# Optimization experiments

Measured on AMD Instinct MI355X. Metric: run time of the kernel, lower is better.

Reference implementation:

```python
import jax, jax.numpy as jnp
import numpy as np

B, S, DIM, H = 8, 4096, 1024, 16
HD = DIM // H
SCALE = HD ** -0.5


def setup_inputs() -> dict:
    key = jax.random.key(0)
    k1, k2, k3 = jax.random.split(key, 3)
    x = jax.random.normal(k1, (B, S, DIM), dtype=jnp.float32)
    # xavier_uniform-ish scales (exact init irrelevant for correctness baseline)
    Wqkv = jax.random.normal(k2, (DIM, 3 * DIM), dtype=jnp.float32) * (2.0 / (DIM + DIM)) ** 0.5
    bqkv = jnp.zeros((3 * DIM,), dtype=jnp.float32)
    Wproj = jax.random.normal(k3, (DIM, DIM), dtype=jnp.float32) * (2.0 / (DIM + DIM)) ** 0.5
    bproj = jnp.zeros((DIM,), dtype=jnp.float32)
    return {"x": x, "Wqkv": Wqkv, "bqkv": bqkv, "Wproj": Wproj, "bproj": bproj}


def reference(x, Wqkv, bqkv, Wproj, bproj):
    b, s, _ = x.shape
    qkv = x @ Wqkv + bqkv                                  # [b, s, 3*dim]
    qkv = qkv.reshape(b, s, 3, H, HD)
    q, k, v = [jnp.transpose(qkv[:, :, i], (0, 2, 1, 3)) for i in range(3)]  # each [b, h, s, hd]
    q = jax.nn.softmax(q, axis=-2) * SCALE                 # softmax over seqlen
    k = jax.nn.softmax(k, axis=-1)                         # softmax over head_dim
    # original computes (k @ v^T)^T @ q; associativity gives v @ (k^T @ q), O(n*d^2)
    A = jnp.einsum("bhtd,bhte->bhde", k, q)                # [b, h, hd, hd]
    out = jnp.einsum("bhsd,bhde->bhse", v, A)              # [b, h, s, hd]
    out = jnp.transpose(out, (0, 2, 1, 3)).reshape(b, s, DIM)
    return out @ Wproj + bproj
```

## Files before the change

### kernel.cpp

```cpp
#include <hip/hip_runtime.h>
#include <hip/hip_bf16.h>

typedef short s16x8 __attribute__((ext_vector_type(8)));
typedef short s16x4 __attribute__((ext_vector_type(4)));
typedef float f32x4 __attribute__((ext_vector_type(4)));
typedef unsigned int u32x4 __attribute__((ext_vector_type(4)));
typedef unsigned int u32x2 __attribute__((ext_vector_type(2)));

__device__ __forceinline__ float b2f(unsigned short u) {
  unsigned int v = ((unsigned int)u) << 16;
  return __builtin_bit_cast(float, v);
}
__device__ __forceinline__ unsigned short f2b(float f) {
  __hip_bfloat16 h = __float2bfloat16(f);
  return __builtin_bit_cast(unsigned short, h);
}
__device__ __forceinline__ void async_ld16(const unsigned short* g, unsigned short* l) {
  __builtin_amdgcn_global_load_lds(
      (const __attribute__((address_space(1))) void*)g,
      (__attribute__((address_space(3))) void*)l, 16, 0, 0);
}

__global__ __launch_bounds__(256) void cast_x_kernel(const float* __restrict__ x,
                                                     unsigned short* __restrict__ xb) {
  int i = (blockIdx.x * 256 + threadIdx.x) * 4;
  f32x4 v = *(const f32x4*)(x + i);
  u32x2 o;
  o[0] = (unsigned)f2b(v[0]) | ((unsigned)f2b(v[1]) << 16);
  o[1] = (unsigned)f2b(v[2]) | ((unsigned)f2b(v[3]) << 16);
  *(u32x2*)(xb + i) = o;
}

__global__ __launch_bounds__(256) void wtrans_kernel(const float* __restrict__ W,
                                                     unsigned short* __restrict__ Wt,
                                                     int K, int N) {
  __shared__ float tile[64][65];
  int n0 = blockIdx.x * 64, k0 = blockIdx.y * 64;
  int tx = threadIdx.x & 63, ty = threadIdx.x >> 6;
  #pragma unroll
  for (int i = ty; i < 64; i += 4) tile[i][tx] = W[(long)(k0 + i) * N + n0 + tx];
  __syncthreads();
  #pragma unroll
  for (int i = ty; i < 64; i += 4) Wt[(long)(n0 + i) * K + k0 + tx] = f2b(tile[tx][i]);
}

template<bool BF16OUT>
__global__ __launch_bounds__(256) void gemm_bt_kernel(
    const unsigned short* __restrict__ A, int lda,
    const unsigned short* __restrict__ Bt0, int ldb,
    const float* __restrict__ bias,
    void* __restrict__ Cv, int N, int K,
    int rows_per_batch, long bstride) {
  __shared__ unsigned short a_lds[128 * 32];
  __shared__ unsigned short b_lds[128 * 32];
  const int tid = threadIdx.x;
  const int lane = tid & 63, wid = tid >> 6;
  const int m0 = blockIdx.y * 128, n0 = blockIdx.x * 128;
  const int wm = (wid >> 1) * 64, wn = (wid & 1) * 64;
  const int fm = lane & 15, fq = lane >> 4;

  const unsigned short* Bt = Bt0;
  if (rows_per_batch) Bt += (long)(m0 / rows_per_batch) * bstride;

  f32x4 acc[4][4] = {};

  const unsigned short* gA[2];
  const unsigned short* gB[2];
  unsigned short* lA[2];
  unsigned short* lB[2];
  #pragma unroll
  for (int j = 0; j < 2; j++) {
    const int C = (wid * 2 + j) * 64 + lane;
    const int r = C >> 2, cp = C & 3;
    const int cg = cp ^ ((r >> 1) & 3);
    gA[j] = A + (long)(m0 + r) * lda + cg * 8;
    gB[j] = Bt + (long)(n0 + r) * ldb + cg * 8;
    lA[j] = a_lds + (wid * 2 + j) * 512;
    lB[j] = b_lds + (wid * 2 + j) * 512;
  }
  const int swa = (fq ^ ((fm >> 1) & 3)) * 8;

  for (int k0 = 0; k0 < K; k0 += 32) {
    __syncthreads();
    async_ld16(gA[0] + k0, lA[0]);
    async_ld16(gA[1] + k0, lA[1]);
    async_ld16(gB[0] + k0, lB[0]);
    async_ld16(gB[1] + k0, lB[1]);
    __syncthreads();
    s16x8 af[4], bfr[4];
    #pragma unroll
    for (int i = 0; i < 4; i++) {
      af[i]  = *(const s16x8*)&a_lds[(wm + i * 16 + fm) * 32 + swa];
      bfr[i] = *(const s16x8*)&b_lds[(wn + i * 16 + fm) * 32 + swa];
    }
    #pragma unroll
    for (int mi = 0; mi < 4; mi++)
      #pragma unroll
      for (int ni = 0; ni < 4; ni++)
        acc[mi][ni] = __builtin_amdgcn_mfma_f32_16x16x32_bf16(af[mi], bfr[ni], acc[mi][ni], 0, 0, 0);
  }

  #pragma unroll
  for (int ni = 0; ni < 4; ni++) {
    const int col = n0 + wn + ni * 16 + fm;
    const float bv = bias[col];
    #pragma unroll
    for (int mi = 0; mi < 4; mi++) {
      #pragma unroll
      for (int r = 0; r < 4; r++) {
        const long row = m0 + wm + mi * 16 + fq * 4 + r;
        const float v = acc[mi][ni][r] + bv;
        if (BF16OUT) ((unsigned short*)Cv)[row * N + col] = f2b(v);
        else         ((float*)Cv)[row * N + col] = v;
      }
    }
  }
}

__global__ __launch_bounds__(256) void apass_kernel(
    const unsigned short* __restrict__ qkv,
    float* __restrict__ Ap,
    float* __restrict__ Dp) {
  __shared__ unsigned short qT[64 * 36 + 8];
  __shared__ unsigned short kT[64 * 36 + 8];
  __shared__ float dled[64];
  const int tid = threadIdx.x;
  const int chunk = blockIdx.x, g = blockIdx.y;
  const int b = g >> 4, h = g & 15;
  const int w = tid >> 6, lane = tid & 63;
  const int fm = lane & 15, fq = lane >> 4;
  const int tl = tid >> 3;
  const int c0 = (tid & 7) * 8;

  if (tid < 64) dled[tid] = 0.f;

  const long row0 = (long)(b * 4096 + chunk * 1024 + tl);
  const unsigned short* qptr = qkv + row0 * 3072 + h * 64 + c0;
  const unsigned short* kptr = qptr + 1024;

  f32x4 acc[4] = {};
  float dacc[8] = {};

  for (int ks = 0; ks < 32; ks++) {
    const long roff = (long)(ks * 32) * 3072;
    u32x4 qv = *(const u32x4*)(qptr + roff);
    u32x4 kv = *(const u32x4*)(kptr + roff);
    float qe[8], ke[8];
    #pragma unroll
    for (int i = 0; i < 4; i++) {
      qe[2*i]   = __expf(b2f((unsigned short)(qv[i] & 0xffffu)));
      qe[2*i+1] = __expf(b2f((unsigned short)(qv[i] >> 16)));
      ke[2*i]   = __expf(b2f((unsigned short)(kv[i] & 0xffffu)));
      ke[2*i+1] = __expf(b2f((unsigned short)(kv[i] >> 16)));
    }
    float p = 0.f;
    #pragma unroll
    for (int i = 0; i < 8; i++) p += ke[i];
    p += __shfl_xor(p, 1);
    p += __shfl_xor(p, 2);
    p += __shfl_xor(p, 4);
    const float kinv = 1.0f / p;
    #pragma unroll
    for (int i = 0; i < 8; i++) dacc[i] += qe[i];
    __syncthreads();
    #pragma unroll
    for (int i = 0; i < 8; i++) {
      qT[(c0 + i) * 36 + tl] = f2b(qe[i] * kinv);
      kT[(c0 + i) * 36 + tl] = f2b(ke[i]);
    }
    __syncthreads();
    const int aoff = (w * 16 + fm) * 36 + fq * 8;
    s16x4 alo = *(const s16x4*)&qT[aoff];
    s16x4 ahi = *(const s16x4*)&qT[aoff + 4];
    s16x8 af = {alo[0], alo[1], alo[2], alo[3], ahi[0], ahi[1], ahi[2], ahi[3]};
    #pragma unroll
    for (int ni = 0; ni < 4; ni++) {
      const int boff = (ni * 16 + fm) * 36 + fq * 8;
      s16x4 blo = *(const s16x4*)&kT[boff];
      s16x4 bhi = *(const s16x4*)&kT[boff + 4];
      s16x8 bfr = {blo[0], blo[1], blo[2], blo[3], bhi[0], bhi[1], bhi[2], bhi[3]};
      acc[ni] = __builtin_amdgcn_mfma_f32_16x16x32_bf16(af, bfr, acc[ni], 0, 0, 0);
    }
  }
  float* ap = Ap + (long)(chunk * 128 + g) * 4096;
  #pragma unroll
  for (int ni = 0; ni < 4; ni++)
    #pragma unroll
    for (int r = 0; r < 4; r++)
      ap[(w * 16 + fq * 4 + r) * 64 + ni * 16 + fm] = acc[ni][r];
  #pragma unroll
  for (int i = 0; i < 8; i++) atomicAdd(&dled[c0 + i], dacc[i]);
  __syncthreads();
  if (tid < 64) Dp[(chunk * 8 + b) * 1024 + h * 64 + tid] = dled[tid];
}

__global__ __launch_bounds__(256) void mmake_kernel(
    const float* __restrict__ Ap,
    const float* __restrict__ Dp,
    const float* __restrict__ Wproj,
    unsigned short* __restrict__ Mt) {
  __shared__ float At[4096];
  __shared__ float Wp[4096];
  const int tid = threadIdx.x;
  const int n0 = blockIdx.x * 64;
  const int g = blockIdx.y;
  const int b = g >> 4, h = g & 15;
  #pragma unroll
  for (int j = 0; j < 16; j++) {
    int lin = tid + 256 * j;
    int e = lin >> 6, n = lin & 63;
    float s = 0.f, den = 0.f;
    #pragma unroll
    for (int c = 0; c < 4; c++) {
      s   += Ap[(long)(c * 128 + g) * 4096 + lin];
      den += Dp[(c * 8 + b) * 1024 + h * 64 + e];
    }
    At[lin] = 0.125f * s / den;
    Wp[lin] = Wproj[(long)(h * 64 + e) * 1024 + n0 + n];
  }
  __syncthreads();
  const int d = tid & 63, ng = tid >> 6;
  float a_reg[64];
  #pragma unroll
  for (int e = 0; e < 64; e++) a_reg[e] = At[e * 64 + d];
  #pragma unroll
  for (int nn = 0; nn < 16; nn++) {
    const int n = ng * 16 + nn;
    float s = 0.f;
    #pragma unroll
    for (int e = 0; e < 64; e++)
      s = fmaf(a_reg[e], Wp[e * 64 + n], s);
    Mt[((long)b << 20) + (long)(n0 + n) * 1024 + h * 64 + d] = f2b(s);
  }
}

extern "C" void kernel_launch(void* const* d_in, const int* in_sizes, int n_in,
                              void* d_out, int out_size, void* d_ws, size_t ws_size,
                              hipStream_t stream) {
  const float* x     = (const float*)d_in[0];
  const float* Wqkv  = (const float*)d_in[1];
  const float* bqkv  = (const float*)d_in[2];
  const float* Wproj = (const float*)d_in[3];
  const float* bproj = (const float*)d_in[4];
  float* out = (float*)d_out;

  char* ws = (char*)d_ws;
  unsigned short* xb  = (unsigned short*)(ws + 0);
  unsigned short* wqt = (unsigned short*)(ws + 67108864);
  unsigned short* qkv = (unsigned short*)(ws + 73400320);
  float*          ap  = (float*)        (ws + 274726912);
  float*          dp  = (float*)        (ws + 283115520);
  unsigned short* mt  = (unsigned short*)(ws + 283246592);

  cast_x_kernel<<<dim3(32768), dim3(256), 0, stream>>>(x, xb);
  wtrans_kernel<<<dim3(48, 16), dim3(256), 0, stream>>>(Wqkv, wqt, 1024, 3072);
  gemm_bt_kernel<true><<<dim3(24, 256), dim3(256), 0, stream>>>(
      xb, 1024, wqt, 1024, bqkv, (void*)qkv, 3072, 1024, 0, 0);
  apass_kernel<<<dim3(4, 128), dim3(256), 0, stream>>>(qkv, ap, dp);
  mmake_kernel<<<dim3(16, 128), dim3(256), 0, stream>>>(ap, dp, Wproj, mt);
  gemm_bt_kernel<false><<<dim3(8, 256), dim3(256), 0, stream>>>(
      qkv + 2048, 3072, mt, 1024, bproj, (void*)out, 1024, 1024, 4096, 1048576);
}
```

Baseline: 729.8 us.

## Replace GEMM with 256x256-tile, 8-wave, double-buffered async-load pipelined kernel

Replaces the 128x128, 4-wave GEMM with a 256x256, 8-wave kernel. It uses a 64-wide K tile, 128 KB of LDS double buffering and an XOR swizzle. Global-to-LDS async loads for future K steps are interleaved with MFMA quarter-blocks, using barriers, s_setprio and vmcnt waits, so that memory latency hides behind compute. Both the QKV projection and the output projection GEMM use it. The larger tiles raise register and LDS pressure, and they depend on dimensions being multiples of 256 and K a multiple of 128.

```diff
diff --git a/kernel.cpp b/kernel.cpp
--- a/kernel.cpp
+++ b/kernel.cpp
@@ -44,72 +44,133 @@
   for (int i = ty; i < 64; i += 4) Wt[(long)(n0 + i) * K + k0 + tx] = f2b(tile[tx][i]);
 }
 
+
+#define BAR() __builtin_amdgcn_s_barrier()
+#define PRIO1() __builtin_amdgcn_s_setprio(1)
+#define PRIO0() __builtin_amdgcn_s_setprio(0)
+#define VMW(n) asm volatile("s_waitcnt vmcnt(" #n ")" ::: "memory")
+
 template<bool BF16OUT>
-__global__ __launch_bounds__(256) void gemm_bt_kernel(
+__global__ __launch_bounds__(512, 2) void gemm8p_kernel(
     const unsigned short* __restrict__ A, int lda,
     const unsigned short* __restrict__ Bt0, int ldb,
     const float* __restrict__ bias,
     void* __restrict__ Cv, int N, int K,
     int rows_per_batch, long bstride) {
-  __shared__ unsigned short a_lds[128 * 32];
-  __shared__ unsigned short b_lds[128 * 32];
+  __shared__ unsigned short lds[65536];
   const int tid = threadIdx.x;
   const int lane = tid & 63, wid = tid >> 6;
-  const int m0 = blockIdx.y * 128, n0 = blockIdx.x * 128;
-  const int wm = (wid >> 1) * 64, wn = (wid & 1) * 64;
+  const int m0 = blockIdx.y * 256, n0 = blockIdx.x * 256;
+  const int wm = (wid >> 2) * 128, wn = (wid & 3) * 64;
   const int fm = lane & 15, fq = lane >> 4;
+  const int kc0 = (fq ^ (fm & 7)) * 8;
+  const int kc1 = kc0 ^ 32;
 
   const unsigned short* Bt = Bt0;
   if (rows_per_batch) Bt += (long)(m0 / rows_per_batch) * bstride;
 
-  f32x4 acc[4][4] = {};
-
-  const unsigned short* gA[2];
-  const unsigned short* gB[2];
-  unsigned short* lA[2];
-  unsigned short* lB[2];
-  #pragma unroll
-  for (int j = 0; j < 2; j++) {
-    const int C = (wid * 2 + j) * 64 + lane;
-    const int r = C >> 2, cp = C & 3;
-    const int cg = cp ^ ((r >> 1) & 3);
-    gA[j] = A + (long)(m0 + r) * lda + cg * 8;
-    gB[j] = Bt + (long)(n0 + r) * ldb + cg * 8;
-    lA[j] = a_lds + (wid * 2 + j) * 512;
-    lB[j] = b_lds + (wid * 2 + j) * 512;
-  }
-  const int swa = (fq ^ ((fm >> 1) & 3)) * 8;
-
-  for (int k0 = 0; k0 < K; k0 += 32) {
-    __syncthreads();
-    async_ld16(gA[0] + k0, lA[0]);
-    async_ld16(gA[1] + k0, lA[1]);
-    async_ld16(gB[0] + k0, lB[0]);
-    async_ld16(gB[1] + k0, lB[1]);
-    __syncthreads();
-    s16x8 af[4], bfr[4];
-    #pragma unroll
-    for (int i = 0; i < 4; i++) {
-      af[i]  = *(const s16x8*)&a_lds[(wm + i * 16 + fm) * 32 + swa];
-      bfr[i] = *(const s16x8*)&b_lds[(wn + i * 16 + fm) * 32 + swa];
-    }
-    #pragma unroll
-    for (int mi = 0; mi < 4; mi++)
-      #pragma unroll
-      for (int ni = 0; ni < 4; ni++)
-        acc[mi][ni] = __builtin_amdgcn_mfma_f32_16x16x32_bf16(af[mi], bfr[ni], acc[mi][ni], 0, 0, 0);
-  }
-
-  #pragma unroll
-  for (int ni = 0; ni < 4; ni++) {
-    const int col = n0 + wn + ni * 16 + fm;
+  const char* sA0; const char* sA1; const char* sB0; const char* sB1;
+  {
+    const int C0 = (wid * 2) * 64 + lane;
+    const int r0 = C0 >> 3, cg0 = (C0 & 7) ^ (r0 & 7);
+    const int C1 = (wid * 2 + 1) * 64 + lane;
+    const int r1 = C1 >> 3, cg1 = (C1 & 7) ^ (r1 & 7);
+    sA0 = (const char*)(A + (long)(m0 + r0) * lda + cg0 * 8);
+    sA1 = (const char*)(A + (long)(m0 + r1) * lda + cg1 * 8);
+    sB0 = (const char*)(Bt + (long)(n0 + r0) * ldb + cg0 * 8);
+    sB1 = (const char*)(Bt + (long)(n0 + r1) * ldb + cg1 * 8);
+  }
+  const long hA = (long)lda * 256;
+  const long hB = (long)ldb * 256;
+  const int ldso = wid * 1024;
+
+#define STG_A(P, h, kt) do { \
+    async_ld16((const unsigned short*)(sA0 + (h) * hA + (long)(kt) * 128), \
+               lds + ((P) * 2 + (h)) * 8192 + ldso); \
+    async_ld16((const unsigned short*)(sA1 + (h) * hA + (long)(kt) * 128), \
+               lds + ((P) * 2 + (h)) * 8192 + ldso + 512); \
+  } while (0)
+#define STG_B(P, h, kt) do { \
+    async_ld16((const unsigned short*)(sB0 + (h) * hB + (long)(kt) * 128), \
+               lds + 32768 + ((P) * 2 + (h)) * 8192 + ldso); \
+    async_ld16((const unsigned short*)(sB1 + (h) * hB + (long)(kt) * 128), \
+               lds + 32768 + ((P) * 2 + (h)) * 8192 + ldso + 512); \
+  } while (0)
+
+  const int aBp0 = (wm >> 7) * 8192;
+  const int aBp1 = 16384 + (wm >> 7) * 8192;
+  const int bBp0 = 32768 + (wn >> 7) * 8192 + (wn & 64) * 64;
+  const int bBp1 = 49152 + (wn >> 7) * 8192 + (wn & 64) * 64;
+
+  s16x8 afr[4][2], bf0[2][2], bf1[2][2];
+  f32x4 acc[8][4] = {};
+
+#define LDA_(base, mq) do { _Pragma("unroll") \
+    for (int mi = 0; mi < 4; mi++) { \
+      const int ro = (base) + (((mq) * 64 + mi * 16 + fm) & 127) * 64; \
+      afr[mi][0] = *(const s16x8*)(lds + ro + kc0); \
+      afr[mi][1] = *(const s16x8*)(lds + ro + kc1); \
+    } } while (0)
+#define LDB_(base, nq, dst) do { _Pragma("unroll") \
+    for (int ni = 0; ni < 2; ni++) { \
+      const int ro = (base) + ((nq) * 32 + ni * 16 + fm) * 64; \
+      dst[ni][0] = *(const s16x8*)(lds + ro + kc0); \
+      dst[ni][1] = *(const s16x8*)(lds + ro + kc1); \
+    } } while (0)
+#define MMQ(mq, nq, bfr) do { _Pragma("unroll") \
+    for (int ks = 0; ks < 2; ks++) { _Pragma("unroll") \
+      for (int mi = 0; mi < 4; mi++) { _Pragma("unroll") \
+        for (int ni = 0; ni < 2; ni++) \
+          acc[(mq) * 4 + mi][(nq) * 2 + ni] = __builtin_amdgcn_mfma_f32_16x16x32_bf16( \
+              afr[mi][ks], bfr[ni][ks], acc[(mq) * 4 + mi][(nq) * 2 + ni], 0, 0, 0); \
+      } } } while (0)
+
+  STG_A(0, 0, 0); STG_A(0, 1, 0); STG_B(0, 0, 0); STG_B(0, 1, 0);
+  STG_B(1, 0, 1); STG_B(1, 1, 1); STG_A(1, 0, 1);
+  VMW(6);
+  BAR();
+
+  const int NIT = K >> 7;
+  #pragma unroll 1
+  for (int i = 0; i < NIT; i++) {
+    const int kt1 = 2 * i + 1, ktE = 2 * i + 2, ktO = 2 * i + 3;
+    const bool st = (i + 1 < NIT);
+    LDA_(aBp0, 0); LDB_(bBp0, 0, bf0);
+    STG_A(1, 1, kt1);
+    BAR(); PRIO1(); MMQ(0, 0, bf0); PRIO0(); BAR();
+    LDB_(bBp0, 1, bf1);
+    BAR(); PRIO1(); MMQ(0, 1, bf1); PRIO0(); BAR();
+    LDA_(aBp0, 1);
+    if (st) { STG_B(0, 0, ktE); STG_B(0, 1, ktE); }
+    BAR(); PRIO1(); MMQ(1, 1, bf1); PRIO0(); BAR();
+    if (st) STG_A(0, 0, ktE);
+    BAR(); PRIO1(); MMQ(1, 0, bf0); PRIO0();
+    if (st) { VMW(6); } else { VMW(0); }
+    BAR();
+    LDA_(aBp1, 0); LDB_(bBp1, 0, bf0);
+    if (st) STG_A(0, 1, ktE);
+    BAR(); PRIO1(); MMQ(0, 0, bf0); PRIO0(); BAR();
+    LDB_(bBp1, 1, bf1);
+    BAR(); PRIO1(); MMQ(0, 1, bf1); PRIO0(); BAR();
+    LDA_(aBp1, 1);
+    if (st) { STG_B(1, 0, ktO); STG_B(1, 1, ktO); }
+    BAR(); PRIO1(); MMQ(1, 1, bf1); PRIO0(); BAR();
+    if (st) STG_A(1, 0, ktO);
+    BAR(); PRIO1(); MMQ(1, 0, bf0); PRIO0();
+    VMW(6);
+    BAR();
+  }
+
+  #pragma unroll
+  for (int ng = 0; ng < 4; ng++) {
+    const int col = n0 + wn + ng * 16 + fm;
     const float bv = bias[col];
     #pragma unroll
-    for (int mi = 0; mi < 4; mi++) {
+    for (int mg = 0; mg < 8; mg++) {
       #pragma unroll
       for (int r = 0; r < 4; r++) {
-        const long row = m0 + wm + mi * 16 + fq * 4 + r;
-        const float v = acc[mi][ni][r] + bv;
+        const long row = m0 + wm + mg * 16 + fq * 4 + r;
+        const float v = acc[mg][ng][r] + bv;
         if (BF16OUT) ((unsigned short*)Cv)[row * N + col] = f2b(v);
         else         ((float*)Cv)[row * N + col] = v;
       }
@@ -254,10 +315,10 @@
 
   cast_x_kernel<<<dim3(32768), dim3(256), 0, stream>>>(x, xb);
   wtrans_kernel<<<dim3(48, 16), dim3(256), 0, stream>>>(Wqkv, wqt, 1024, 3072);
-  gemm_bt_kernel<true><<<dim3(24, 256), dim3(256), 0, stream>>>(
+  gemm8p_kernel<true><<<dim3(12, 128), dim3(512), 0, stream>>>(
       xb, 1024, wqt, 1024, bqkv, (void*)qkv, 3072, 1024, 0, 0);
   apass_kernel<<<dim3(4, 128), dim3(256), 0, stream>>>(qkv, ap, dp);
   mmake_kernel<<<dim3(16, 128), dim3(256), 0, stream>>>(ap, dp, Wproj, mt);
-  gemm_bt_kernel<false><<<dim3(8, 256), dim3(256), 0, stream>>>(
+  gemm8p_kernel<false><<<dim3(4, 128), dim3(512), 0, stream>>>(
       qkv + 2048, 3072, mt, 1024, bproj, (void*)out, 1024, 1024, 4096, 1048576);
 }
```

Result: faster. 657.6 us (-9.9%).
